# Kernel optimization log

Hardware: AMD Instinct MI355X
Metric: run time of the kernel (lower is better)

Reference implementation:

```python
import jax, jax.numpy as jnp
import numpy as np

NUM_HEADS = 8
HEAD_DIM = 16  # d_model=128 / 8 heads
SCALE = HEAD_DIM ** -0.5


def setup_inputs() -> dict:
    key = jax.random.key(0)
    ks = jax.random.split(key, 12)
    B, A, K, L, D, M = 8, 64, 16, 30, 128, 128
    s = 1.0 / np.sqrt(D)
    inp = {
        "future_feat": jax.random.normal(ks[0], (B, A, L, D), jnp.float32),
        "geom_bias": jax.random.normal(ks[1], (B, A, K), jnp.float32),
        "Wq": jax.random.normal(ks[2], (D, M), jnp.float32) * s,
        "bq": jnp.zeros((M,), jnp.float32),
        "Wk": jax.random.normal(ks[3], (D, M), jnp.float32) * s,
        "bk": jnp.zeros((M,), jnp.float32),
        "Wv": jax.random.normal(ks[4], (D, M), jnp.float32) * s,
        "bv": jnp.zeros((M,), jnp.float32),
        "Wo": jax.random.normal(ks[5], (M, M), jnp.float32) * s,
        "bo": jnp.zeros((M,), jnp.float32),
        "neighbour_indices": jax.random.randint(ks[6], (B, A, K), 0, A),
        "neighbour_mask": jax.random.randint(ks[7], (B, A, K), 0, 2).astype(bool),
    }
    return inp


def reference(future_feat, geom_bias, Wq, bq, Wk, bk, Wv, bv, Wo, bo,
              neighbour_indices, neighbour_mask):
    B, A, L, D = future_feat.shape
    K = neighbour_indices.shape[2]
    H, HD = NUM_HEADS, HEAD_DIM

    # gather neighbour futures: [B, A, K, L, D]
    neighbours = jax.vmap(lambda f, idx: f[idx])(future_feat, neighbour_indices)

    q = (future_feat @ Wq + bq).reshape(B, A, L, H, HD).transpose(0, 1, 3, 2, 4)      # [B,A,H,Lq,hd]
    k = (neighbours @ Wk + bk).reshape(B, A, K, L, H, HD).transpose(0, 1, 4, 2, 3, 5)  # [B,A,H,K,Lk,hd]
    v = (neighbours @ Wv + bv).reshape(B, A, K, L, H, HD).transpose(0, 1, 4, 2, 3, 5)  # [B,A,H,K,Lk,hd]

    scores = jnp.einsum('bahqd,bahkld->bahqkl', q, k) * SCALE                          # [B,A,H,Lq,K,Lk]
    scores = scores + geom_bias[:, :, None, None, :, None]
    scores = jnp.where(neighbour_mask[:, :, None, None, :, None], scores, -jnp.inf)

    attn = jax.nn.softmax(scores.reshape(B, A, H, L, K * L), axis=-1)
    attn = jnp.nan_to_num(attn).reshape(B, A, H, L, K, L)

    ctx = jnp.einsum('bahqkl,bahkld->bahqd', attn, v)                                  # [B,A,H,Lq,hd]
    ctx = ctx.transpose(0, 1, 3, 2, 4).reshape(B, A, L, H * HD)
    out = ctx @ Wo + bo                                                                # [B,A,Lq,d_model]
    return out, attn
```

## Files before the change

kernel.cpp:

```cpp
#include <hip/hip_runtime.h>
#include <math.h>


#define NB 8
#define NA 64
#define NK 16
#define NL 30
#define ND 128
#define NM 128
#define NH 8
#define NHD 16
#define NKK (NK*NL)
#define FSCALE 0.25f
#define NROWS (NB*NA*NL)

typedef __attribute__((ext_vector_type(8))) short bf16x8;
typedef __attribute__((ext_vector_type(4))) float f32x4;

__device__ __forceinline__ unsigned short bf16r(float x) {
    unsigned u = __float_as_uint(x);
    return (unsigned short)((u + 0x7fffu + ((u >> 16) & 1u)) >> 16);
}
__device__ __forceinline__ float bf16tof(unsigned short h) {
    return __uint_as_float((unsigned)h << 16);
}

__global__ __launch_bounds__(256) void prep_kernel(
    const float* __restrict__ Wq, const float* __restrict__ Wk,
    const float* __restrict__ Wv, const float* __restrict__ Wo,
    const float* __restrict__ bq, const float* __restrict__ bk,
    const float* __restrict__ bv, const float* __restrict__ bo,
    const unsigned int* __restrict__ nmask_u, int* __restrict__ mflag,
    short* __restrict__ WtH, short* __restrict__ WtL, float* __restrict__ bias_ws)
{
    const int t = threadIdx.x;
    if (blockIdx.x == 8) {
        __shared__ int not_i32, not_f32;
        if (t == 0) { not_i32 = 0; not_f32 = 0; }
        __syncthreads();
        for (int i = t; i < 2048; i += 256) {
            unsigned u = nmask_u[i];
            if (u > 1u) not_i32 = 1;
            if (u != 0u && u != 0x3F800000u) not_f32 = 1;
        }
        __syncthreads();
        if (t == 0) *mflag = (!not_i32) ? 0 : ((!not_f32) ? 1 : 2);
        if (t < 128) {
            bias_ws[t]       = bq[t];
            bias_ws[128 + t] = bk[t];
            bias_ws[256 + t] = bv[t];
            bias_ws[384 + t] = bo[t];
        }
        return;
    }
    const int m = blockIdx.x >> 1, half = blockIdx.x & 1, d0 = half * 64;
    const float* W = (m == 0) ? Wq : (m == 1) ? Wk : (m == 2) ? Wv : Wo;
    __shared__ __align__(16) float xs[64][132];
    for (int i = t; i < 2048; i += 256) {
        const int dd = i >> 5, j4 = (i & 31) * 4;
        *(float4*)&xs[dd][j4] = *(const float4*)(W + (size_t)(d0 + dd) * NM + j4);
    }
    __syncthreads();
    const int n = t >> 1, hs = t & 1;
    unsigned short hb[32], lb[32];
    #pragma unroll
    for (int s = 0; s < 32; ++s) {
        float v = xs[hs*32 + s][n];
        unsigned short h = bf16r(v);
        hb[s] = h;
        lb[s] = bf16r(v - bf16tof(h));
    }
    const size_t base = (size_t)m * 16384 + (size_t)n * 128 + d0 + hs * 32;
    #pragma unroll
    for (int g = 0; g < 8; ++g) {
        unsigned long long ph =
              (unsigned long long)hb[4*g]
            | ((unsigned long long)hb[4*g+1] << 16)
            | ((unsigned long long)hb[4*g+2] << 32)
            | ((unsigned long long)hb[4*g+3] << 48);
        unsigned long long pl =
              (unsigned long long)lb[4*g]
            | ((unsigned long long)lb[4*g+1] << 16)
            | ((unsigned long long)lb[4*g+2] << 32)
            | ((unsigned long long)lb[4*g+3] << 48);
        *(unsigned long long*)(WtH + base + g*4) = ph;
        *(unsigned long long*)(WtL + base + g*4) = pl;
    }
}

__global__ __launch_bounds__(256, 3) void proj_mfma(
    const float* X,
    const short* __restrict__ WtH, const short* __restrict__ WtL,
    const float* __restrict__ bias_ws,
    float* Y, int mat_off)
{
    const int m    = blockIdx.y;
    const int mi   = mat_off + m;
    const int rt   = blockIdx.x;
    const int t    = threadIdx.x;
    const int lane = t & 63, w = t >> 6;
    const int n    = lane & 15, quad = lane >> 4;

    const short* wh = WtH + (size_t)mi * 16384 + (size_t)n * 128 + quad * 8;
    const short* wl = WtL + (size_t)mi * 16384 + (size_t)n * 128 + quad * 8;

    const int arow = rt*64 + w*16 + n;
    const float* xr = X + (size_t)arow * ND + quad*8;
    bf16x8 Ah[4], Al[4];
    #pragma unroll
    for (int ks = 0; ks < 4; ++ks) {
        float4 x0 = *(const float4*)(xr + ks*32);
        float4 x1 = *(const float4*)(xr + ks*32 + 4);
        float xv[8] = {x0.x,x0.y,x0.z,x0.w,x1.x,x1.y,x1.z,x1.w};
        #pragma unroll
        for (int j = 0; j < 8; ++j) {
            unsigned short h = bf16r(xv[j]);
            Ah[ks][j] = (short)h;
            Al[ks][j] = (short)bf16r(xv[j] - bf16tof(h));
        }
    }

    float* yb = Y + (size_t)m * NROWS * NM
                  + (size_t)(rt*64 + w*16 + quad*4) * NM + n;
    #pragma unroll 2
    for (int nt = 0; nt < 8; ++nt) {
        f32x4 acc = {0.f, 0.f, 0.f, 0.f};
        #pragma unroll
        for (int ks = 0; ks < 4; ++ks) {
            bf16x8 bh = *(const bf16x8*)(wh + nt*2048 + ks*32);
            bf16x8 bl = *(const bf16x8*)(wl + nt*2048 + ks*32);
            acc = __builtin_amdgcn_mfma_f32_16x16x32_bf16(Ah[ks], bh, acc, 0, 0, 0);
            acc = __builtin_amdgcn_mfma_f32_16x16x32_bf16(Al[ks], bh, acc, 0, 0, 0);
            acc = __builtin_amdgcn_mfma_f32_16x16x32_bf16(Ah[ks], bl, acc, 0, 0, 0);
        }
        const float bn = bias_ws[mi*128 + nt*16 + n];
        #pragma unroll
        for (int r = 0; r < 4; ++r)
            yb[(size_t)r * NM + nt*16] = acc[r] + bn;
    }
}

__global__ __launch_bounds__(128, 2) void attn_kernel(
    const float* __restrict__ qp, const float* __restrict__ kp, const float* __restrict__ vp,
    const float* __restrict__ geom_bias, const int* __restrict__ nidx,
    const void* __restrict__ nmask, const int* __restrict__ mask_fmt,
    float* __restrict__ attn_out, float* __restrict__ ctx_out)
{
    __shared__ __align__(16) short Kbf[NKK][16];
    __shared__ __align__(16) short Vt[16][488];
    __shared__ __align__(16) short pbuf[2][16][40];
    __shared__ __align__(16) float pf[2][16][36];
    __shared__ float bias_ext[NKK];
    __shared__ float biasm[NK];
    __shared__ int   idx_s[NK];

    const int t    = threadIdx.x;
    const int blk  = blockIdx.x;
    const int h    = blk & 7;
    const int ba   = blk >> 3;
    const int b    = ba >> 6;
    const int lane = t & 63;
    const int w    = t >> 6;
    const int n    = lane & 15;
    const int quad = lane >> 4;

    if (t < NK) {
        idx_s[t] = nidx[ba*NK + t];
        const int fmt = *mask_fmt;
        bool mv;
        if (fmt == 0)      mv = ((const int*)nmask)[ba*NK + t] != 0;
        else if (fmt == 1) mv = ((const float*)nmask)[ba*NK + t] != 0.0f;
        else               mv = ((const unsigned char*)nmask)[ba*NK + t] != 0;
        biasm[t] = mv ? geom_bias[ba*NK + t] : -INFINITY;
    }
    __syncthreads();

    for (int i = t; i < NKK*4; i += 128) {
        const int kk = i >> 2, p = i & 3;
        const int kn = kk / NL, l = kk - kn*NL;
        const size_t off = ((size_t)(b*NA + idx_s[kn])*NL + l)*NM + h*NHD + p*4;
        float4 kv = *(const float4*)(kp + off);
        unsigned long long pk =
              (unsigned long long)bf16r(kv.x)
            | ((unsigned long long)bf16r(kv.y) << 16)
            | ((unsigned long long)bf16r(kv.z) << 32)
            | ((unsigned long long)bf16r(kv.w) << 48);
        *(unsigned long long*)&Kbf[kk][p*4] = pk;
        float4 vv = *(const float4*)(vp + off);
        Vt[p*4+0][kk] = (short)bf16r(vv.x);
        Vt[p*4+1][kk] = (short)bf16r(vv.y);
        Vt[p*4+2][kk] = (short)bf16r(vv.z);
        Vt[p*4+3][kk] = (short)bf16r(vv.w);
    }
    for (int i = t; i < NKK; i += 128) bias_ext[i] = biasm[i / NL];

    bf16x8 a_hi, a_lo;
    #pragma unroll
    for (int j = 0; j < 8; ++j) { a_hi[j] = 0; a_lo[j] = 0; }
    const int qrow = w*16 + n;
    if (quad < 2 && qrow < NL) {
        const float* qb = qp + ((size_t)ba*NL + qrow)*NM + h*NHD + quad*8;
        float4 x0 = *(const float4*)(qb);
        float4 x1 = *(const float4*)(qb + 4);
        float xv[8] = {x0.x,x0.y,x0.z,x0.w,x1.x,x1.y,x1.z,x1.w};
        #pragma unroll
        for (int j = 0; j < 8; ++j) {
            float x = xv[j] * FSCALE;
            unsigned short hbv = bf16r(x);
            a_hi[j] = (short)hbv;
            a_lo[j] = (short)bf16r(x - bf16tof(hbv));
        }
    }
    __syncthreads();

    float s[NL][4];
    #pragma unroll
    for (int tt = 0; tt < NL; ++tt) {
        bf16x8 bfrag;
        #pragma unroll
        for (int j = 0; j < 8; ++j) bfrag[j] = 0;
        if (quad < 2)
            bfrag = *(const bf16x8*)&Kbf[tt*16 + n][quad*8];
        f32x4 acc = {0.f, 0.f, 0.f, 0.f};
        acc = __builtin_amdgcn_mfma_f32_16x16x32_bf16(a_hi, bfrag, acc, 0, 0, 0);
        acc = __builtin_amdgcn_mfma_f32_16x16x32_bf16(a_lo, bfrag, acc, 0, 0, 0);
        const float bv = bias_ext[tt*16 + n];
        s[tt][0] = acc[0] + bv;
        s[tt][1] = acc[1] + bv;
        s[tt][2] = acc[2] + bv;
        s[tt][3] = acc[3] + bv;
    }

    #pragma unroll
    for (int r = 0; r < 4; ++r) {
        float m = -INFINITY;
        #pragma unroll
        for (int tt = 0; tt < NL; ++tt) m = fmaxf(m, s[tt][r]);
        m = fmaxf(m, __shfl_xor(m, 1));
        m = fmaxf(m, __shfl_xor(m, 2));
        m = fmaxf(m, __shfl_xor(m, 4));
        m = fmaxf(m, __shfl_xor(m, 8));
        const bool ok = (m > -INFINITY);
        float sum = 0.f;
        #pragma unroll
        for (int tt = 0; tt < NL; ++tt) {
            float p = ok ? __expf(s[tt][r] - m) : 0.f;
            s[tt][r] = p;
            sum += p;
        }
        sum += __shfl_xor(sum, 1);
        sum += __shfl_xor(sum, 2);
        sum += __shfl_xor(sum, 4);
        sum += __shfl_xor(sum, 8);
        const float inv = (sum > 0.f) ? 1.f / sum : 0.f;
        #pragma unroll
        for (int tt = 0; tt < NL; ++tt) s[tt][r] *= inv;
    }

    const size_t abase = (size_t)blk * NL * NKK;
    const int rr = lane >> 2, seg = lane & 3;
    const int qr_st = w*16 + rr;
    f32x4 ctx = {0.f, 0.f, 0.f, 0.f};
    #pragma unroll
    for (int c = 0; c < 15; ++c) {
        #pragma unroll
        for (int r = 0; r < 4; ++r) {
            const float p0 = s[2*c][r], p1 = s[2*c + 1][r];
            pbuf[w][quad*4 + r][n]      = (short)bf16r(p0);
            pbuf[w][quad*4 + r][16 + n] = (short)bf16r(p1);
            pf[w][quad*4 + r][n]        = p0;
            pf[w][quad*4 + r][16 + n]   = p1;
        }
        bf16x8 pa = *(const bf16x8*)&pbuf[w][n][quad*8];
        bf16x8 vb = *(const bf16x8*)&Vt[n][c*32 + quad*8];
        ctx = __builtin_amdgcn_mfma_f32_16x16x32_bf16(pa, vb, ctx, 0, 0, 0);
        if (qr_st < NL) {
            float4 o0 = *(const float4*)&pf[w][rr][seg*8 + 0];
            float4 o1 = *(const float4*)&pf[w][rr][seg*8 + 4];
            float* ap = attn_out + abase + (size_t)qr_st*NKK + c*32 + seg*8;
            *(float4*)ap       = o0;
            *(float4*)(ap + 4) = o1;
        }
    }

    #pragma unroll
    for (int r = 0; r < 4; ++r) {
        const int qr = w*16 + quad*4 + r;
        if (qr < NL)
            ctx_out[((size_t)ba*NL + qr)*NM + h*NHD + n] = ctx[r];
    }
}

extern "C" void kernel_launch(void* const* d_in, const int* in_sizes, int n_in,
                              void* d_out, int out_size, void* d_ws, size_t ws_size,
                              hipStream_t stream)
{
    const float* x    = (const float*)d_in[0];
    const float* gb   = (const float*)d_in[1];
    const float* Wq   = (const float*)d_in[2];
    const float* bq   = (const float*)d_in[3];
    const float* Wk   = (const float*)d_in[4];
    const float* bk   = (const float*)d_in[5];
    const float* Wv   = (const float*)d_in[6];
    const float* bv   = (const float*)d_in[7];
    const float* Wo   = (const float*)d_in[8];
    const float* bo   = (const float*)d_in[9];
    const int*   nidx = (const int*)d_in[10];
    const void*  nmask= d_in[11];

    float* out  = (float*)d_out;
    float* attn = out + (size_t)NROWS * NM;

    float* qp = (float*)d_ws;
    float* kp = qp + (size_t)NROWS * NM;
    float* vp = kp + (size_t)NROWS * NM;
    int*   mflag   = (int*)(vp + (size_t)NROWS * NM);
    float* bias_ws = (float*)(mflag + 4);
    short* WtH     = (short*)(bias_ws + 512);
    short* WtL     = WtH + 4 * 16384;

    prep_kernel<<<9, 256, 0, stream>>>(Wq, Wk, Wv, Wo, bq, bk, bv, bo,
                                       (const unsigned int*)nmask, mflag,
                                       WtH, WtL, bias_ws);
    dim3 gproj(NROWS/64, 3);
    proj_mfma<<<gproj, 256, 0, stream>>>(x, WtH, WtL, bias_ws, qp, 0);
    attn_kernel<<<NB*NA*NH, 128, 0, stream>>>(qp, kp, vp, gb, nidx, nmask, mflag,
                                              attn,  out);
    dim3 gout(NROWS/64, 1);
    proj_mfma<<<gout, 256, 0, stream>>>(out, WtH, WtL, bias_ws, out, 3);
}
```

Baseline: 377.0 us.

## Transpose attention MFMA layout to keep softmax rows in-lane and drop LDS staging

Switches the score and context MFMAs to the 16x16x16 bf16 form with K as the A operand and Q as B. Each lane now holds whole query-row values, so the softmax reduction needs only two cross-quad shuffles, and probabilities feed the PV MFMA straight from registers. This drops the pbuf/pf LDS round trips, and attn rows are written as float4 directly. It also removes the first syncthreads by reading indices and mask from global memory, and remaps block IDs to spread heads across the grid. In exchange it issues twice as many MFMA instructions, and the attn stores become strided per lane.

```diff
diff --git a/kernel.cpp b/kernel.cpp
--- a/kernel.cpp
+++ b/kernel.cpp
@@ -15,6 +15,7 @@
 #define NROWS (NB*NA*NL)
 
 typedef __attribute__((ext_vector_type(8))) short bf16x8;
+typedef __attribute__((ext_vector_type(4))) short bf16x4;
 typedef __attribute__((ext_vector_type(4))) float f32x4;
 
 __device__ __forceinline__ unsigned short bf16r(float x) {
@@ -23,6 +24,17 @@
 }
 __device__ __forceinline__ float bf16tof(unsigned short h) {
     return __uint_as_float((unsigned)h << 16);
+}
+
+__device__ __forceinline__ f32x4 mfma16(bf16x4 a, bf16x4 b, f32x4 c) {
+#if __has_builtin(__builtin_amdgcn_mfma_f32_16x16x16bf16_1k)
+    return __builtin_amdgcn_mfma_f32_16x16x16bf16_1k(a, b, c, 0, 0, 0);
+#else
+    f32x4 d;
+    asm("v_mfma_f32_16x16x16_bf16 %0, %1, %2, %3"
+        : "=&v"(d) : "v"(a), "v"(b), "v"(c));
+    return d;
+#endif
 }
 
 __global__ __launch_bounds__(256) void prep_kernel(
@@ -147,15 +159,12 @@
     float* __restrict__ attn_out, float* __restrict__ ctx_out)
 {
     __shared__ __align__(16) short Kbf[NKK][16];
-    __shared__ __align__(16) short Vt[16][488];
-    __shared__ __align__(16) short pbuf[2][16][40];
-    __shared__ __align__(16) float pf[2][16][36];
-    __shared__ float bias_ext[NKK];
-    __shared__ float biasm[NK];
-    __shared__ int   idx_s[NK];
+    __shared__ __align__(16) short Vt[16][484];
+    __shared__ __align__(16) float bias_ext[NKK];
 
     const int t    = threadIdx.x;
-    const int blk  = blockIdx.x;
+    const int bid  = blockIdx.x;
+    const int blk  = (bid & 7) * ((NB*NA*NH) >> 3) + (bid >> 3);
     const int h    = blk & 7;
     const int ba   = blk >> 3;
     const int b    = ba >> 6;
@@ -164,21 +173,11 @@
     const int n    = lane & 15;
     const int quad = lane >> 4;
 
-    if (t < NK) {
-        idx_s[t] = nidx[ba*NK + t];
-        const int fmt = *mask_fmt;
-        bool mv;
-        if (fmt == 0)      mv = ((const int*)nmask)[ba*NK + t] != 0;
-        else if (fmt == 1) mv = ((const float*)nmask)[ba*NK + t] != 0.0f;
-        else               mv = ((const unsigned char*)nmask)[ba*NK + t] != 0;
-        biasm[t] = mv ? geom_bias[ba*NK + t] : -INFINITY;
-    }
-    __syncthreads();
-
     for (int i = t; i < NKK*4; i += 128) {
         const int kk = i >> 2, p = i & 3;
         const int kn = kk / NL, l = kk - kn*NL;
-        const size_t off = ((size_t)(b*NA + idx_s[kn])*NL + l)*NM + h*NHD + p*4;
+        const int nb = nidx[ba*NK + kn];
+        const size_t off = ((size_t)(b*NA + nb)*NL + l)*NM + h*NHD + p*4;
         float4 kv = *(const float4*)(kp + off);
         unsigned long long pk =
               (unsigned long long)bf16r(kv.x)
@@ -192,23 +191,30 @@
         Vt[p*4+2][kk] = (short)bf16r(vv.z);
         Vt[p*4+3][kk] = (short)bf16r(vv.w);
     }
-    for (int i = t; i < NKK; i += 128) bias_ext[i] = biasm[i / NL];
-
-    bf16x8 a_hi, a_lo;
-    #pragma unroll
-    for (int j = 0; j < 8; ++j) { a_hi[j] = 0; a_lo[j] = 0; }
+    {
+        const int fmt = *mask_fmt;
+        for (int i = t; i < NKK; i += 128) {
+            const int kn = i / NL;
+            bool mv;
+            if (fmt == 0)      mv = ((const int*)nmask)[ba*NK + kn] != 0;
+            else if (fmt == 1) mv = ((const float*)nmask)[ba*NK + kn] != 0.0f;
+            else               mv = ((const unsigned char*)nmask)[ba*NK + kn] != 0;
+            bias_ext[i] = mv ? geom_bias[ba*NK + kn] : -INFINITY;
+        }
+    }
+
+    bf16x4 q_hi = {0,0,0,0}, q_lo = {0,0,0,0};
     const int qrow = w*16 + n;
-    if (quad < 2 && qrow < NL) {
-        const float* qb = qp + ((size_t)ba*NL + qrow)*NM + h*NHD + quad*8;
-        float4 x0 = *(const float4*)(qb);
-        float4 x1 = *(const float4*)(qb + 4);
-        float xv[8] = {x0.x,x0.y,x0.z,x0.w,x1.x,x1.y,x1.z,x1.w};
-        #pragma unroll
-        for (int j = 0; j < 8; ++j) {
-            float x = xv[j] * FSCALE;
-            unsigned short hbv = bf16r(x);
-            a_hi[j] = (short)hbv;
-            a_lo[j] = (short)bf16r(x - bf16tof(hbv));
+    if (qrow < NL) {
+        const float* qb = qp + ((size_t)ba*NL + qrow)*NM + h*NHD + quad*4;
+        float4 x = *(const float4*)qb;
+        float xv[4] = {x.x, x.y, x.z, x.w};
+        #pragma unroll
+        for (int j = 0; j < 4; ++j) {
+            float xs = xv[j] * FSCALE;
+            unsigned short hv = bf16r(xs);
+            q_hi[j] = (short)hv;
+            q_lo[j] = (short)bf16r(xs - bf16tof(hv));
         }
     }
     __syncthreads();
@@ -216,78 +222,56 @@
     float s[NL][4];
     #pragma unroll
     for (int tt = 0; tt < NL; ++tt) {
-        bf16x8 bfrag;
-        #pragma unroll
-        for (int j = 0; j < 8; ++j) bfrag[j] = 0;
-        if (quad < 2)
-            bfrag = *(const bf16x8*)&Kbf[tt*16 + n][quad*8];
+        bf16x4 kf = *(const bf16x4*)&Kbf[tt*16 + n][quad*4];
         f32x4 acc = {0.f, 0.f, 0.f, 0.f};
-        acc = __builtin_amdgcn_mfma_f32_16x16x32_bf16(a_hi, bfrag, acc, 0, 0, 0);
-        acc = __builtin_amdgcn_mfma_f32_16x16x32_bf16(a_lo, bfrag, acc, 0, 0, 0);
-        const float bv = bias_ext[tt*16 + n];
-        s[tt][0] = acc[0] + bv;
-        s[tt][1] = acc[1] + bv;
-        s[tt][2] = acc[2] + bv;
-        s[tt][3] = acc[3] + bv;
-    }
-
-    #pragma unroll
-    for (int r = 0; r < 4; ++r) {
-        float m = -INFINITY;
-        #pragma unroll
-        for (int tt = 0; tt < NL; ++tt) m = fmaxf(m, s[tt][r]);
-        m = fmaxf(m, __shfl_xor(m, 1));
-        m = fmaxf(m, __shfl_xor(m, 2));
-        m = fmaxf(m, __shfl_xor(m, 4));
-        m = fmaxf(m, __shfl_xor(m, 8));
-        const bool ok = (m > -INFINITY);
-        float sum = 0.f;
-        #pragma unroll
-        for (int tt = 0; tt < NL; ++tt) {
-            float p = ok ? __expf(s[tt][r] - m) : 0.f;
+        acc = mfma16(kf, q_hi, acc);
+        acc = mfma16(kf, q_lo, acc);
+        const f32x4 bv = *(const f32x4*)&bias_ext[tt*16 + quad*4];
+        #pragma unroll
+        for (int r = 0; r < 4; ++r) s[tt][r] = acc[r] + bv[r];
+    }
+
+    float mx = -INFINITY;
+    #pragma unroll
+    for (int tt = 0; tt < NL; ++tt)
+        #pragma unroll
+        for (int r = 0; r < 4; ++r) mx = fmaxf(mx, s[tt][r]);
+    mx = fmaxf(mx, __shfl_xor(mx, 16));
+    mx = fmaxf(mx, __shfl_xor(mx, 32));
+    const bool okr = (mx > -INFINITY);
+    float sum = 0.f;
+    #pragma unroll
+    for (int tt = 0; tt < NL; ++tt) {
+        #pragma unroll
+        for (int r = 0; r < 4; ++r) {
+            float p = okr ? __expf(s[tt][r] - mx) : 0.f;
             s[tt][r] = p;
             sum += p;
         }
-        sum += __shfl_xor(sum, 1);
-        sum += __shfl_xor(sum, 2);
-        sum += __shfl_xor(sum, 4);
-        sum += __shfl_xor(sum, 8);
-        const float inv = (sum > 0.f) ? 1.f / sum : 0.f;
-        #pragma unroll
-        for (int tt = 0; tt < NL; ++tt) s[tt][r] *= inv;
-    }
-
-    const size_t abase = (size_t)blk * NL * NKK;
-    const int rr = lane >> 2, seg = lane & 3;
-    const int qr_st = w*16 + rr;
+    }
+    sum += __shfl_xor(sum, 16);
+    sum += __shfl_xor(sum, 32);
+    const float inv = (sum > 0.f) ? 1.f / sum : 0.f;
+
+    float* arow = attn_out + (size_t)blk * NL * NKK + (size_t)qrow * NKK;
     f32x4 ctx = {0.f, 0.f, 0.f, 0.f};
     #pragma unroll
-    for (int c = 0; c < 15; ++c) {
-        #pragma unroll
-        for (int r = 0; r < 4; ++r) {
-            const float p0 = s[2*c][r], p1 = s[2*c + 1][r];
-            pbuf[w][quad*4 + r][n]      = (short)bf16r(p0);
-            pbuf[w][quad*4 + r][16 + n] = (short)bf16r(p1);
-            pf[w][quad*4 + r][n]        = p0;
-            pf[w][quad*4 + r][16 + n]   = p1;
-        }
-        bf16x8 pa = *(const bf16x8*)&pbuf[w][n][quad*8];
-        bf16x8 vb = *(const bf16x8*)&Vt[n][c*32 + quad*8];
-        ctx = __builtin_amdgcn_mfma_f32_16x16x32_bf16(pa, vb, ctx, 0, 0, 0);
-        if (qr_st < NL) {
-            float4 o0 = *(const float4*)&pf[w][rr][seg*8 + 0];
-            float4 o1 = *(const float4*)&pf[w][rr][seg*8 + 4];
-            float* ap = attn_out + abase + (size_t)qr_st*NKK + c*32 + seg*8;
-            *(float4*)ap       = o0;
-            *(float4*)(ap + 4) = o1;
-        }
-    }
-
-    #pragma unroll
-    for (int r = 0; r < 4; ++r) {
-        const int qr = w*16 + quad*4 + r;
-        if (qr < NL)
-            ctx_out[((size_t)ba*NL + qr)*NM + h*NHD + n] = ctx[r];
+    for (int tt = 0; tt < NL; ++tt) {
+        const float p0 = s[tt][0]*inv, p1 = s[tt][1]*inv;
+        const float p2 = s[tt][2]*inv, p3 = s[tt][3]*inv;
+        if (qrow < NL) {
+            float4 o = {p0, p1, p2, p3};
+            *(float4*)(arow + tt*16 + quad*4) = o;
+        }
+        bf16x4 pb;
+        pb[0] = (short)bf16r(p0); pb[1] = (short)bf16r(p1);
+        pb[2] = (short)bf16r(p2); pb[3] = (short)bf16r(p3);
+        bf16x4 vf = *(const bf16x4*)&Vt[n][tt*16 + quad*4];
+        ctx = mfma16(vf, pb, ctx);
+    }
+    if (qrow < NL) {
+        float4 c = {ctx[0], ctx[1], ctx[2], ctx[3]};
+        *(float4*)(ctx_out + ((size_t)ba*NL + qrow)*NM + h*NHD + quad*4) = c;
     }
 }
 
```

Measured after the change: 355.7 us. 5.7% less time.
